# Kernel optimization log

Measured on AMD Instinct MI355X. Metric: run time of the kernel, lower is better.

Reference implementation:

```python
import jax, jax.numpy as jnp
import numpy as np

S = 512            # sample_points along each ray
VD = VH = VW = 128  # voxel volume shape (drr.density.shape)
DET = 128           # detector H = W


def setup_inputs() -> dict:
    key = jax.random.key(0)
    k1, k2, k3 = jax.random.split(key, 3)
    B = 2
    pred_frontal = jax.random.uniform(k1, (B, 1, DET, DET), dtype=jnp.float32)
    pred_lateral = jax.random.uniform(k2, (B, 1, DET, DET), dtype=jnp.float32)
    ii, jj = jnp.meshgrid(jnp.arange(DET, dtype=jnp.float32),
                          jnp.arange(DET, dtype=jnp.float32), indexing='ij')
    # frontal: source behind volume on -z, detector plane at z=328
    source_F = jnp.array([[64.0, 64.0, -200.0]], dtype=jnp.float32)
    target_F = jnp.stack([ii, jj, jnp.full_like(ii, 328.0)], axis=-1)[None]  # (1,H,W,3)
    # lateral: source on -x, detector plane at x=328
    source_L = jnp.array([[-200.0, 64.0, 64.0]], dtype=jnp.float32)
    target_L = jnp.stack([jnp.full_like(ii, 328.0), ii, jj], axis=-1)[None]
    vol_gt_3d = jax.random.uniform(k3, (VD, VH, VW), dtype=jnp.float32)
    A_inv = jnp.eye(3, dtype=jnp.float32)   # drr.affine_inverse linear part
    t_inv = jnp.zeros(3, dtype=jnp.float32)  # drr.affine_inverse translation
    return {"pred_frontal": pred_frontal, "pred_lateral": pred_lateral,
            "source_F": source_F, "target_F": target_F,
            "source_L": source_L, "target_L": target_L,
            "vol_gt_3d": vol_gt_3d, "A_inv": A_inv, "t_inv": t_inv}


def _backproject(mask_2d, src, target_grid, A_inv, t_inv, threshold=0.5):
    # mask_2d: (H,W); src: (3,); target_grid: (H,W,3)
    active = (mask_2d > threshold).reshape(-1)          # (P,) bool
    det_pixels = target_grid.reshape(-1, 3)             # (P,3)
    ray_dirs = det_pixels - src[None, :]                 # (P,3)
    ray_len = jnp.linalg.norm(ray_dirs, axis=1, keepdims=True)  # (P,1)
    ray_dirs = ray_dirs / (ray_len + 1e-8)
    t_vals = jnp.linspace(0.0, 1.0, S, dtype=mask_2d.dtype)[None, :, None]  # (1,S,1)
    t_samples = t_vals * (ray_len[:, None, :] * 2.5)     # (P,S,1)
    world_pts = src[None, None, :] + ray_dirs[:, None, :] * t_samples  # (P,S,3)
    voxel = jnp.round(world_pts @ A_inv.T + t_inv).astype(jnp.int32)   # (P,S,3)
    valid = (active[:, None]
             & (voxel[..., 0] >= 0) & (voxel[..., 0] < VD)
             & (voxel[..., 1] >= 0) & (voxel[..., 1] < VH)
             & (voxel[..., 2] >= 0) & (voxel[..., 2] < VW))
    vi = jnp.clip(voxel, 0, jnp.array([VD - 1, VH - 1, VW - 1], dtype=jnp.int32))
    vol = jnp.zeros((VD, VH, VW), dtype=mask_2d.dtype)
    # set-to-1 scatter: max with {0,1} values; invalid samples write 0 (no-op)
    vol = vol.at[vi[..., 0], vi[..., 1], vi[..., 2]].max(valid.astype(mask_2d.dtype))
    return vol


def reference(pred_frontal, pred_lateral, source_F, target_F,
              source_L, target_L, vol_gt_3d, A_inv, t_inv):
    src_F, tgt_F = source_F[0], target_F[0]
    src_L, tgt_L = source_L[0], target_L[0]
    B = pred_frontal.shape[0]
    total = jnp.zeros((), dtype=pred_frontal.dtype)
    for i in range(B):
        vol_F = _backproject(pred_frontal[i, 0], src_F, tgt_F, A_inv, t_inv)
        vol_L = _backproject(pred_lateral[i, 0], src_L, tgt_L, A_inv, t_inv)
        p = jax.nn.sigmoid(vol_F + vol_L)  # values in sigmoid({0,1,2})
        bce = -jnp.mean(vol_gt_3d * jnp.log(p) + (1.0 - vol_gt_3d) * jnp.log1p(-p))
        total = total + bce
    return total / B
```

## Files before the change

### kernel.cpp

```cpp
#include <hip/hip_runtime.h>

#define DETN 128
#define NPIX (DETN * DETN)
#define VDIM 128
#define NVOX (VDIM * VDIM * VDIM)
#define NWORDS (NVOX / 32)
#define NSAMP 512
#define SPLITK 4

__global__ __launch_bounds__(256) void bp_kernel(
    const float* __restrict__ predF, const float* __restrict__ predL,
    const float* __restrict__ srcF,  const float* __restrict__ srcL,
    const float* __restrict__ tgtF,  const float* __restrict__ tgtL,
    const float* __restrict__ Ainv,  const float* __restrict__ tinv,
    unsigned int* __restrict__ flags, float* __restrict__ out)
{
    if (blockIdx.x == 0 && blockIdx.y == 0 && blockIdx.z == 0 &&
        threadIdx.x == 0) {
        *out = 0.0f;
    }

    const int p     = blockIdx.y;
    const int view  = p & 1;
    const int batch = p >> 1;
    const int ray   = blockIdx.x * blockDim.x + threadIdx.x;

    const float* mask = (view ? predL : predF) + batch * NPIX;
    if (!(mask[ray] > 0.5f)) return;

    const float* src = view ? srcL : srcF;
    const float* tgt = (view ? tgtL : tgtF) + ray * 3;

    const float sx = src[0], sy = src[1], sz = src[2];
    float dx = tgt[0] - sx, dy = tgt[1] - sy, dz = tgt[2] - sz;
    const float len = sqrtf(dx * dx + dy * dy + dz * dz);
    const float inv = 1.0f / (len + 1e-8f);
    dx *= inv; dy *= inv; dz *= inv;

    const float a00 = Ainv[0], a01 = Ainv[1], a02 = Ainv[2];
    const float a10 = Ainv[3], a11 = Ainv[4], a12 = Ainv[5];
    const float a20 = Ainv[6], a21 = Ainv[7], a22 = Ainv[8];
    const float qcx = a00 * sx + a01 * sy + a02 * sz + tinv[0];
    const float qcy = a10 * sx + a11 * sy + a12 * sz + tinv[1];
    const float qcz = a20 * sx + a21 * sy + a22 * sz + tinv[2];
    const float qdx = a00 * dx + a01 * dy + a02 * dz;
    const float qdy = a10 * dx + a11 * dy + a12 * dz;
    const float qdz = a20 * dx + a21 * dy + a22 * dz;

    const float tmax = len * 2.5f;
    const float dt   = tmax * (1.0f / 511.0f);

    float tlo = 0.0f, thi = tmax;
    {
        const float c[3] = {qcx, qcy, qcz};
        const float d[3] = {qdx, qdy, qdz};
        #pragma unroll
        for (int j = 0; j < 3; ++j) {
            if (fabsf(d[j]) < 1e-8f) {
                if (c[j] < -0.6f || c[j] > 127.6f) thi = -1.0f;
            } else {
                const float ta = (-0.6f  - c[j]) / d[j];
                const float tb = (127.6f - c[j]) / d[j];
                tlo = fmaxf(tlo, fminf(ta, tb));
                thi = fminf(thi, fmaxf(ta, tb));
            }
        }
    }
    if (tlo > thi) return;
    const int klo = max(0, (int)ceilf(tlo / dt));
    const int khi = min(NSAMP - 1, (int)floorf(thi / dt));

    const int n   = khi - klo + 1;
    const int per = (n + SPLITK - 1) / SPLITK;
    const int k0  = klo + (int)blockIdx.z * per;
    const int k1  = min(khi, k0 + per - 1);
    if (k0 > khi) return;

    unsigned int* __restrict__ vol = flags + (size_t)p * NWORDS;
    int      curw = -1;
    unsigned bits = 0;
    for (int k = k0; k <= k1; ++k) {
        const float t  = (float)k * dt;
        const float qx = fmaf(qdx, t, qcx);
        const float qy = fmaf(qdy, t, qcy);
        const float qz = fmaf(qdz, t, qcz);
        const int ix = (int)rintf(qx);
        const int iy = (int)rintf(qy);
        const int iz = (int)rintf(qz);
        if ((unsigned)ix < (unsigned)VDIM && (unsigned)iy < (unsigned)VDIM &&
            (unsigned)iz < (unsigned)VDIM) {
            const int maj = view ? iz : ix;
            const int pk  = view ? ix : iz;
            const int w   = (maj << 9) | (iy << 2) | (pk >> 5);
            const unsigned bit = 1u << (pk & 31);
            if (w == curw) {
                bits |= bit;
            } else {
                if (curw >= 0) atomicOr(&vol[curw], bits);
                curw = w; bits = bit;
            }
        }
    }
    if (curw >= 0) atomicOr(&vol[curw], bits);
}

__global__ __launch_bounds__(256) void loss_kernel(
    const unsigned int* __restrict__ flags,
    const float* __restrict__ gt,
    float* __restrict__ out, float scale)
{
    __shared__ unsigned latw[2][2][128];
    __shared__ unsigned fst[2][256];
    __shared__ float    smem[4];

    const int X0 = blockIdx.x & 3;
    const int y0 = (blockIdx.x >> 2) << 1;
    const int tid = threadIdx.x;

    #pragma unroll
    for (int b = 0; b < 2; ++b) {
        {
            const int r  = tid;
            const int yi = r >> 7;
            const int z  = r & 127;
            latw[b][yi][z] =
                flags[(size_t)(2 * b + 1) * NWORDS + (z << 9) + ((y0 + yi) << 2) + X0];
        }
        {
            const int r  = tid;
            const int xi = r >> 3;
            const int yi = (r >> 2) & 1;
            const int Zi = r & 3;
            fst[b][r] =
                flags[(size_t)(2 * b) * NWORDS + ((32 * X0 + xi) << 9) +
                      ((y0 + yi) << 2) + Zi];
        }
    }
    __syncthreads();

    const int xi = tid & 31;
    const int yi = (tid >> 5) & 1;
    const int Zi = tid >> 6;
    const int w  = ((32 * X0 + xi) << 9) | ((y0 + yi) << 2) | Zi;

    const float4* __restrict__ g4 = (const float4*)(gt + (size_t)w * 32);
    float g[32];
    #pragma unroll
    for (int q = 0; q < 8; ++q) {
        const float4 v = g4[q];
        g[4 * q + 0] = v.x; g[4 * q + 1] = v.y;
        g[4 * q + 2] = v.z; g[4 * q + 3] = v.w;
    }

    float acc = 0.0f;
    #pragma unroll
    for (int b = 0; b < 2; ++b) {
        const unsigned F = fst[b][(xi << 3) | (yi << 2) | Zi];
        unsigned L = 0;
        #pragma unroll
        for (int zz = 0; zz < 32; ++zz) {
            L |= ((latw[b][yi][(Zi << 5) + zz] >> xi) & 1u) << zz;
        }
        const int n2 = __popc(F & L);
        const int n1 = __popc(F | L) - n2;
        const int n0 = 32 - n1 - n2;
        acc += 0.6931471806f * (float)n0 + 1.3132616875f * (float)n1 +
               2.1269280110f * (float)n2;
        float s = 0.0f;
        #pragma unroll
        for (int i = 0; i < 32; ++i) {
            s += g[i] * (float)(((F >> i) & 1u) + ((L >> i) & 1u));
        }
        acc -= s;
    }

    #pragma unroll
    for (int off = 32; off > 0; off >>= 1) acc += __shfl_down(acc, off);

    const int wid  = tid >> 6;
    const int lane = tid & 63;
    if (lane == 0) smem[wid] = acc;
    __syncthreads();
    if (tid == 0) {
        const float tot = smem[0] + smem[1] + smem[2] + smem[3];
        atomicAdd(out, tot * scale);
    }
}

extern "C" void kernel_launch(void* const* d_in, const int* in_sizes, int n_in,
                              void* d_out, int out_size, void* d_ws, size_t ws_size,
                              hipStream_t stream) {
    const float* predF = (const float*)d_in[0];
    const float* predL = (const float*)d_in[1];
    const float* srcF  = (const float*)d_in[2];
    const float* tgtF  = (const float*)d_in[3];
    const float* srcL  = (const float*)d_in[4];
    const float* tgtL  = (const float*)d_in[5];
    const float* gt    = (const float*)d_in[6];
    const float* Ainv  = (const float*)d_in[7];
    const float* tinv  = (const float*)d_in[8];

    const int B = in_sizes[0] / NPIX;
    unsigned int* flags = (unsigned int*)d_ws;
    float* outp = (float*)d_out;

    hipMemsetAsync(flags, 0, (size_t)(2 * B) * NWORDS * sizeof(unsigned int), stream);

    dim3 gridBp(NPIX / 256, 2 * B, SPLITK);
    bp_kernel<<<gridBp, 256, 0, stream>>>(predF, predL, srcF, srcL,
                                          tgtF, tgtL, Ainv, tinv, flags, outp);

    const float scale = 1.0f / ((float)NVOX * (float)B);
    loss_kernel<<<256, 256, 0, stream>>>(flags, gt, outp, scale);
}
```

Measured before the change: 111.4 us.

## Fuse memset, backprojection and loss into one cooperative kernel with grid syncs

Replaces the memset plus two kernel launches with a single cooperative kernel of 1024 blocks that zeroes the flag volume, runs the backprojection, and computes the loss, separated by grid-wide syncs. The loss stage now splits work across 512 blocks, one batch each, and builds the lateral bit words with a shuffle-based 32x32 bit transpose instead of a serial 32-iteration gather loop. This is meant to remove launch and memset overhead and shorten the loss stage. In exchange it depends on all 1024 blocks being co-resident and pays for two grid barriers. The memset also hardcodes 4 volumes, which assumes B=2.

```diff
diff --git a/kernel.cpp b/kernel.cpp
--- a/kernel.cpp
+++ b/kernel.cpp
@@ -1,4 +1,7 @@
 #include <hip/hip_runtime.h>
+#include <hip/hip_cooperative_groups.h>
+
+namespace cg = cooperative_groups;
 
 #define DETN 128
 #define NPIX (DETN * DETN)
@@ -7,183 +10,195 @@
 #define NWORDS (NVOX / 32)
 #define NSAMP 512
 #define SPLITK 4
-
-__global__ __launch_bounds__(256) void bp_kernel(
+#define NBLK 1024
+
+__global__ __launch_bounds__(256, 4) void fused_kernel(
     const float* __restrict__ predF, const float* __restrict__ predL,
     const float* __restrict__ srcF,  const float* __restrict__ srcL,
     const float* __restrict__ tgtF,  const float* __restrict__ tgtL,
     const float* __restrict__ Ainv,  const float* __restrict__ tinv,
-    unsigned int* __restrict__ flags, float* __restrict__ out)
-{
-    if (blockIdx.x == 0 && blockIdx.y == 0 && blockIdx.z == 0 &&
-        threadIdx.x == 0) {
-        *out = 0.0f;
-    }
-
-    const int p     = blockIdx.y;
-    const int view  = p & 1;
-    const int batch = p >> 1;
-    const int ray   = blockIdx.x * blockDim.x + threadIdx.x;
-
-    const float* mask = (view ? predL : predF) + batch * NPIX;
-    if (!(mask[ray] > 0.5f)) return;
-
-    const float* src = view ? srcL : srcF;
-    const float* tgt = (view ? tgtL : tgtF) + ray * 3;
-
-    const float sx = src[0], sy = src[1], sz = src[2];
-    float dx = tgt[0] - sx, dy = tgt[1] - sy, dz = tgt[2] - sz;
-    const float len = sqrtf(dx * dx + dy * dy + dz * dz);
-    const float inv = 1.0f / (len + 1e-8f);
-    dx *= inv; dy *= inv; dz *= inv;
-
-    const float a00 = Ainv[0], a01 = Ainv[1], a02 = Ainv[2];
-    const float a10 = Ainv[3], a11 = Ainv[4], a12 = Ainv[5];
-    const float a20 = Ainv[6], a21 = Ainv[7], a22 = Ainv[8];
-    const float qcx = a00 * sx + a01 * sy + a02 * sz + tinv[0];
-    const float qcy = a10 * sx + a11 * sy + a12 * sz + tinv[1];
-    const float qcz = a20 * sx + a21 * sy + a22 * sz + tinv[2];
-    const float qdx = a00 * dx + a01 * dy + a02 * dz;
-    const float qdy = a10 * dx + a11 * dy + a12 * dz;
-    const float qdz = a20 * dx + a21 * dy + a22 * dz;
-
-    const float tmax = len * 2.5f;
-    const float dt   = tmax * (1.0f / 511.0f);
-
-    float tlo = 0.0f, thi = tmax;
-    {
-        const float c[3] = {qcx, qcy, qcz};
-        const float d[3] = {qdx, qdy, qdz};
-        #pragma unroll
-        for (int j = 0; j < 3; ++j) {
-            if (fabsf(d[j]) < 1e-8f) {
-                if (c[j] < -0.6f || c[j] > 127.6f) thi = -1.0f;
-            } else {
-                const float ta = (-0.6f  - c[j]) / d[j];
-                const float tb = (127.6f - c[j]) / d[j];
-                tlo = fmaxf(tlo, fminf(ta, tb));
-                thi = fminf(thi, fmaxf(ta, tb));
-            }
-        }
-    }
-    if (tlo > thi) return;
-    const int klo = max(0, (int)ceilf(tlo / dt));
-    const int khi = min(NSAMP - 1, (int)floorf(thi / dt));
-
-    const int n   = khi - klo + 1;
-    const int per = (n + SPLITK - 1) / SPLITK;
-    const int k0  = klo + (int)blockIdx.z * per;
-    const int k1  = min(khi, k0 + per - 1);
-    if (k0 > khi) return;
-
-    unsigned int* __restrict__ vol = flags + (size_t)p * NWORDS;
-    int      curw = -1;
-    unsigned bits = 0;
-    for (int k = k0; k <= k1; ++k) {
-        const float t  = (float)k * dt;
-        const float qx = fmaf(qdx, t, qcx);
-        const float qy = fmaf(qdy, t, qcy);
-        const float qz = fmaf(qdz, t, qcz);
-        const int ix = (int)rintf(qx);
-        const int iy = (int)rintf(qy);
-        const int iz = (int)rintf(qz);
-        if ((unsigned)ix < (unsigned)VDIM && (unsigned)iy < (unsigned)VDIM &&
-            (unsigned)iz < (unsigned)VDIM) {
-            const int maj = view ? iz : ix;
-            const int pk  = view ? ix : iz;
-            const int w   = (maj << 9) | (iy << 2) | (pk >> 5);
-            const unsigned bit = 1u << (pk & 31);
-            if (w == curw) {
-                bits |= bit;
-            } else {
-                if (curw >= 0) atomicOr(&vol[curw], bits);
-                curw = w; bits = bit;
-            }
-        }
-    }
-    if (curw >= 0) atomicOr(&vol[curw], bits);
-}
-
-__global__ __launch_bounds__(256) void loss_kernel(
-    const unsigned int* __restrict__ flags,
+    unsigned int* __restrict__ flags,
     const float* __restrict__ gt,
     float* __restrict__ out, float scale)
 {
-    __shared__ unsigned latw[2][2][128];
-    __shared__ unsigned fst[2][256];
+    __shared__ unsigned latw[2][128];
+    __shared__ unsigned fst[256];
     __shared__ float    smem[4];
 
-    const int X0 = blockIdx.x & 3;
-    const int y0 = (blockIdx.x >> 2) << 1;
+    cg::grid_group grid = cg::this_grid();
     const int tid = threadIdx.x;
 
-    #pragma unroll
-    for (int b = 0; b < 2; ++b) {
+    {
+        const int gid = blockIdx.x * 256 + tid;
+        flags[gid] = 0u;
+        if (gid == 0) *out = 0.0f;
+    }
+    grid.sync();
+
+    {
+        const int p    = (blockIdx.x >> 6) & 3;
+        const int view = p & 1;
+        const int batch= p >> 1;
+        const int zs   = blockIdx.x >> 8;
+        const int ray  = (blockIdx.x & 63) * 256 + tid;
+
+        const float* mask = (view ? predL : predF) + batch * NPIX;
+        if (mask[ray] > 0.5f) {
+            const float* src = view ? srcL : srcF;
+            const float* tgt = (view ? tgtL : tgtF) + ray * 3;
+
+            const float sx = src[0], sy = src[1], sz = src[2];
+            float dx = tgt[0] - sx, dy = tgt[1] - sy, dz = tgt[2] - sz;
+            const float len = sqrtf(dx * dx + dy * dy + dz * dz);
+            const float inv = 1.0f / (len + 1e-8f);
+            dx *= inv; dy *= inv; dz *= inv;
+
+            const float a00 = Ainv[0], a01 = Ainv[1], a02 = Ainv[2];
+            const float a10 = Ainv[3], a11 = Ainv[4], a12 = Ainv[5];
+            const float a20 = Ainv[6], a21 = Ainv[7], a22 = Ainv[8];
+            const float qcx = a00 * sx + a01 * sy + a02 * sz + tinv[0];
+            const float qcy = a10 * sx + a11 * sy + a12 * sz + tinv[1];
+            const float qcz = a20 * sx + a21 * sy + a22 * sz + tinv[2];
+            const float qdx = a00 * dx + a01 * dy + a02 * dz;
+            const float qdy = a10 * dx + a11 * dy + a12 * dz;
+            const float qdz = a20 * dx + a21 * dy + a22 * dz;
+
+            const float tmax = len * 2.5f;
+            const float dt   = tmax * (1.0f / 511.0f);
+
+            float tlo = 0.0f, thi = tmax;
+            {
+                const float c[3] = {qcx, qcy, qcz};
+                const float d[3] = {qdx, qdy, qdz};
+                #pragma unroll
+                for (int j = 0; j < 3; ++j) {
+                    if (fabsf(d[j]) < 1e-8f) {
+                        if (c[j] < -0.6f || c[j] > 127.6f) thi = -1.0f;
+                    } else {
+                        const float ta = (-0.6f  - c[j]) / d[j];
+                        const float tb = (127.6f - c[j]) / d[j];
+                        tlo = fmaxf(tlo, fminf(ta, tb));
+                        thi = fminf(thi, fmaxf(ta, tb));
+                    }
+                }
+            }
+            if (tlo <= thi) {
+                const int klo = max(0, (int)ceilf(tlo / dt));
+                const int khi = min(NSAMP - 1, (int)floorf(thi / dt));
+                const int n   = khi - klo + 1;
+                const int per = (n + SPLITK - 1) / SPLITK;
+                const int k0  = klo + zs * per;
+                const int k1  = min(khi, k0 + per - 1);
+                if (k0 <= khi) {
+                    unsigned int* __restrict__ vol = flags + (size_t)p * NWORDS;
+                    int      curw = -1;
+                    unsigned bits = 0;
+                    for (int k = k0; k <= k1; ++k) {
+                        const float t  = (float)k * dt;
+                        const float qx = fmaf(qdx, t, qcx);
+                        const float qy = fmaf(qdy, t, qcy);
+                        const float qz = fmaf(qdz, t, qcz);
+                        const int ix = (int)rintf(qx);
+                        const int iy = (int)rintf(qy);
+                        const int iz = (int)rintf(qz);
+                        if ((unsigned)ix < (unsigned)VDIM &&
+                            (unsigned)iy < (unsigned)VDIM &&
+                            (unsigned)iz < (unsigned)VDIM) {
+                            const int maj = view ? iz : ix;
+                            const int pk  = view ? ix : iz;
+                            const int w   = (maj << 9) | (iy << 2) | (pk >> 5);
+                            const unsigned bit = 1u << (pk & 31);
+                            if (w == curw) {
+                                bits |= bit;
+                            } else {
+                                if (curw >= 0) atomicOr(&vol[curw], bits);
+                                curw = w; bits = bit;
+                            }
+                        }
+                    }
+                    if (curw >= 0) atomicOr(&vol[curw], bits);
+                }
+            }
+        }
+    }
+    grid.sync();
+
+    if (blockIdx.x < 512) {
+        const int b  = blockIdx.x & 1;
+        const int X0 = (blockIdx.x >> 1) & 3;
+        const int y0 = (blockIdx.x >> 3) << 1;
+
         {
-            const int r  = tid;
-            const int yi = r >> 7;
-            const int z  = r & 127;
-            latw[b][yi][z] =
+            const int yi = tid >> 7;
+            const int z  = tid & 127;
+            latw[yi][z] =
                 flags[(size_t)(2 * b + 1) * NWORDS + (z << 9) + ((y0 + yi) << 2) + X0];
-        }
+
+            const int xi2 = tid >> 3;
+            const int yi2 = (tid >> 2) & 1;
+            const int Zi2 = tid & 3;
+            fst[tid] =
+                flags[(size_t)(2 * b) * NWORDS + ((32 * X0 + xi2) << 9) +
+                      ((y0 + yi2) << 2) + Zi2];
+        }
+        __syncthreads();
+
+        const int xi   = tid & 31;
+        const int yi   = (tid >> 5) & 1;
+        const int Zi   = tid >> 6;
+        const int lane = tid & 63;
+
+        unsigned W = latw[lane >> 5][(Zi << 5) | (lane & 31)];
         {
-            const int r  = tid;
-            const int xi = r >> 3;
-            const int yi = (r >> 2) & 1;
-            const int Zi = r & 3;
-            fst[b][r] =
-                flags[(size_t)(2 * b) * NWORDS + ((32 * X0 + xi) << 9) +
-                      ((y0 + yi) << 2) + Zi];
-        }
-    }
-    __syncthreads();
-
-    const int xi = tid & 31;
-    const int yi = (tid >> 5) & 1;
-    const int Zi = tid >> 6;
-    const int w  = ((32 * X0 + xi) << 9) | ((y0 + yi) << 2) | Zi;
-
-    const float4* __restrict__ g4 = (const float4*)(gt + (size_t)w * 32);
-    float g[32];
-    #pragma unroll
-    for (int q = 0; q < 8; ++q) {
-        const float4 v = g4[q];
-        g[4 * q + 0] = v.x; g[4 * q + 1] = v.y;
-        g[4 * q + 2] = v.z; g[4 * q + 3] = v.w;
-    }
-
-    float acc = 0.0f;
-    #pragma unroll
-    for (int b = 0; b < 2; ++b) {
-        const unsigned F = fst[b][(xi << 3) | (yi << 2) | Zi];
-        unsigned L = 0;
-        #pragma unroll
-        for (int zz = 0; zz < 32; ++zz) {
-            L |= ((latw[b][yi][(Zi << 5) + zz] >> xi) & 1u) << zz;
-        }
+            unsigned o;
+            o = __shfl_xor(W, 1);
+            W = (lane & 1)  ? ((W & 0xAAAAAAAAu) | ((o & 0xAAAAAAAAu) >> 1))
+                            : ((W & 0x55555555u) | ((o & 0x55555555u) << 1));
+            o = __shfl_xor(W, 2);
+            W = (lane & 2)  ? ((W & 0xCCCCCCCCu) | ((o & 0xCCCCCCCCu) >> 2))
+                            : ((W & 0x33333333u) | ((o & 0x33333333u) << 2));
+            o = __shfl_xor(W, 4);
+            W = (lane & 4)  ? ((W & 0xF0F0F0F0u) | ((o & 0xF0F0F0F0u) >> 4))
+                            : ((W & 0x0F0F0F0Fu) | ((o & 0x0F0F0F0Fu) << 4));
+            o = __shfl_xor(W, 8);
+            W = (lane & 8)  ? ((W & 0xFF00FF00u) | ((o & 0xFF00FF00u) >> 8))
+                            : ((W & 0x00FF00FFu) | ((o & 0x00FF00FFu) << 8));
+            o = __shfl_xor(W, 16);
+            W = (lane & 16) ? ((W & 0xFFFF0000u) | ((o & 0xFFFF0000u) >> 16))
+                            : ((W & 0x0000FFFFu) | ((o & 0x0000FFFFu) << 16));
+        }
+        const unsigned L = W;
+        const unsigned F = fst[(xi << 3) | (yi << 2) | Zi];
+
         const int n2 = __popc(F & L);
         const int n1 = __popc(F | L) - n2;
         const int n0 = 32 - n1 - n2;
-        acc += 0.6931471806f * (float)n0 + 1.3132616875f * (float)n1 +
-               2.1269280110f * (float)n2;
-        float s = 0.0f;
+
+        const int w = ((32 * X0 + xi) << 9) | ((y0 + yi) << 2) | Zi;
+        const float4* __restrict__ g4 = (const float4*)(gt + ((size_t)w << 5));
+        float sdot = 0.0f;
         #pragma unroll
-        for (int i = 0; i < 32; ++i) {
-            s += g[i] * (float)(((F >> i) & 1u) + ((L >> i) & 1u));
-        }
-        acc -= s;
-    }
-
-    #pragma unroll
-    for (int off = 32; off > 0; off >>= 1) acc += __shfl_down(acc, off);
-
-    const int wid  = tid >> 6;
-    const int lane = tid & 63;
-    if (lane == 0) smem[wid] = acc;
-    __syncthreads();
-    if (tid == 0) {
-        const float tot = smem[0] + smem[1] + smem[2] + smem[3];
-        atomicAdd(out, tot * scale);
+        for (int q = 0; q < 8; ++q) {
+            const float4 v = g4[q];
+            const int i0 = q << 2;
+            sdot += v.x * (float)(((F >> (i0 + 0)) & 1u) + ((L >> (i0 + 0)) & 1u));
+            sdot += v.y * (float)(((F >> (i0 + 1)) & 1u) + ((L >> (i0 + 1)) & 1u));
+            sdot += v.z * (float)(((F >> (i0 + 2)) & 1u) + ((L >> (i0 + 2)) & 1u));
+            sdot += v.w * (float)(((F >> (i0 + 3)) & 1u) + ((L >> (i0 + 3)) & 1u));
+        }
+
+        float acc = 0.6931471806f * (float)n0 + 1.3132616875f * (float)n1 +
+                    2.1269280110f * (float)n2 - sdot;
+
+        #pragma unroll
+        for (int off = 32; off > 0; off >>= 1) acc += __shfl_down(acc, off);
+        const int wid = tid >> 6;
+        if ((tid & 63) == 0) smem[wid] = acc;
+        __syncthreads();
+        if (tid == 0) {
+            const float tot = smem[0] + smem[1] + smem[2] + smem[3];
+            atomicAdd(out, tot * scale);
+        }
     }
 }
 
@@ -203,13 +218,10 @@
     const int B = in_sizes[0] / NPIX;
     unsigned int* flags = (unsigned int*)d_ws;
     float* outp = (float*)d_out;
-
-    hipMemsetAsync(flags, 0, (size_t)(2 * B) * NWORDS * sizeof(unsigned int), stream);
-
-    dim3 gridBp(NPIX / 256, 2 * B, SPLITK);
-    bp_kernel<<<gridBp, 256, 0, stream>>>(predF, predL, srcF, srcL,
-                                          tgtF, tgtL, Ainv, tinv, flags, outp);
-
-    const float scale = 1.0f / ((float)NVOX * (float)B);
-    loss_kernel<<<256, 256, 0, stream>>>(flags, gt, outp, scale);
+    float scale = 1.0f / ((float)NVOX * (float)B);
+
+    void* args[] = {&predF, &predL, &srcF, &srcL, &tgtF, &tgtL,
+                    &Ainv, &tinv, &flags, &gt, &outp, &scale};
+    hipLaunchCooperativeKernel((void*)fused_kernel, dim3(NBLK), dim3(256),
+                               args, 0, stream);
 }
```

Result: slower. 287.2 us (+157.8%).
